# Kernel tuning notes

Measured on AMD Instinct MI355X. Metric: run time of the kernel, lower is better.

## Reference

```python
import jax, jax.numpy as jnp
import numpy as np

N, E, D, H = 50000, 800000, 128, 4
DH = D // H  # head dim = 32


def setup_inputs() -> dict:
    key = jax.random.key(0)
    ks = jax.random.split(key, 16)
    inp = {
        "node_feats": jax.random.normal(ks[0], (N, D), jnp.float32),
        "edge_feats": jax.random.normal(ks[1], (E, D), jnp.float32),
        "src": jax.random.randint(ks[2], (E,), 0, N, jnp.int32),
        "dst": jax.random.randint(ks[3], (E,), 0, N, jnp.int32),
        # MHA projections (no bias since num_input == num_output feats)
        "Wq": jax.random.normal(ks[4], (D, D), jnp.float32) / np.sqrt(D),
        "Wk": jax.random.normal(ks[5], (D, D), jnp.float32) / np.sqrt(D),
        "Wv": jax.random.normal(ks[6], (D, D), jnp.float32) / np.sqrt(D),
        "We": jax.random.normal(ks[7], (D, D), jnp.float32) / np.sqrt(D),
        # output projection (with bias)
        "O_w": jax.random.normal(ks[8], (D, D), jnp.float32) / np.sqrt(D),
        "O_b": jnp.zeros((D,), jnp.float32),
        # batch-norm affine params
        "g1n": jnp.ones((D,), jnp.float32), "b1n": jnp.zeros((D,), jnp.float32),
        "g1e": jnp.ones((D,), jnp.float32), "b1e": jnp.zeros((D,), jnp.float32),
        "g2": jnp.ones((D,), jnp.float32), "b2": jnp.zeros((D,), jnp.float32),
        # node-feats MLP (no bias)
        "W1": jax.random.normal(ks[9], (D, 2 * D), jnp.float32) / np.sqrt(D),
        "W2": jax.random.normal(ks[10], (2 * D, D), jnp.float32) / np.sqrt(2 * D),
    }
    return inp


def _batch_norm(x, gamma, beta, eps=1e-5):
    # training-style BatchNorm1d: biased variance over the batch (node/edge) dim
    mean = jnp.mean(x, axis=0)
    var = jnp.var(x, axis=0)
    return (x - mean) * jax.lax.rsqrt(var + eps) * gamma + beta


def reference(node_feats, edge_feats, src, dst, Wq, Wk, Wv, We, O_w, O_b,
              g1n, b1n, g1e, b1e, g2, b2, W1, W2):
    h_in1 = node_feats
    nf = _batch_norm(node_feats, g1n, b1n)
    ef = _batch_norm(edge_feats, g1e, b1e)

    Q = (nf @ Wq).reshape(N, H, DH)
    K = (nf @ Wk).reshape(N, H, DH)
    V = (nf @ Wv).reshape(N, H, DH)
    proj_e = (ef @ We).reshape(E, H, DH)

    # edge-wise multiplicative attention: [E, H, DH]
    score = jnp.clip(K[src] * Q[dst] / np.sqrt(DH).astype(np.float32), -5.0, 5.0) * proj_e
    s = jnp.exp(jnp.clip(jnp.sum(score, axis=-1, keepdims=True), -5.0, 5.0))  # [E, H, 1]

    # scatter-sum aggregation to destination nodes
    wV = jax.ops.segment_sum(s * V[src], dst, num_segments=N)  # [N, H, DH]
    z = jax.ops.segment_sum(s, dst, num_segments=N)            # [N, H, 1]
    h = (wV / (z + 1e-6)).reshape(N, D)

    # dropout is identity in eval mode
    h = h @ O_w + O_b
    h = h_in1 + h  # residual 1

    h_in2 = h
    h = _batch_norm(h, g2, b2)
    h = jax.nn.silu(h @ W1) @ W2  # node_feats_MLP (dropout = identity)
    h = h_in2 + h  # residual 2
    return h
```

## Files before the change

kernel.cpp:

```cpp
#include <hip/hip_runtime.h>
#include <hip/hip_bf16.h>
#include <math.h>

#define N_NODES 50000
#define N_EDGES 800000
#define DIM 128
#define NH 4

typedef __attribute__((ext_vector_type(8))) short bf16x8;
typedef __attribute__((ext_vector_type(4))) float f32x4;
typedef unsigned int uint;
typedef unsigned short ushort;

__device__ inline short f2bf(float f) {
  __hip_bfloat16 h = __float2bfloat16(f);
  return __builtin_bit_cast(short, h);
}
__device__ inline uint pack_bf2(float lo, float hi) {
  return (uint)(ushort)f2bf(lo) | ((uint)(ushort)f2bf(hi) << 16);
}
__device__ inline float bflo(uint u) { return __builtin_bit_cast(float, u << 16); }
__device__ inline float bfhi(uint u) { return __builtin_bit_cast(float, u & 0xffff0000u); }

__global__ __launch_bounds__(256) void stats_all_kernel(
    const float* __restrict__ nf, const float* __restrict__ ef,
    const int* __restrict__ dst,
    float* __restrict__ stats_n, float* __restrict__ stats_e,
    int* __restrict__ deg, ushort* __restrict__ efb) {
  __shared__ float s_sum[DIM];
  __shared__ float s_sq[DIM];
  int t = threadIdx.x;
  if (t < DIM) { s_sum[t] = 0.f; s_sq[t] = 0.f; }
  __syncthreads();
  int c4 = (t & 31) * 4;
  int rg = t >> 5;
  float sum0=0,sum1=0,sum2=0,sum3=0, sq0=0,sq1=0,sq2=0,sq3=0;
  if (blockIdx.x < 512) {
    for (long row = (long)blockIdx.x * 8 + rg; row < N_NODES; row += 512L * 8) {
      float4 v = *reinterpret_cast<const float4*>(nf + row * DIM + c4);
      sum0 += v.x; sq0 += v.x * v.x;
      sum1 += v.y; sq1 += v.y * v.y;
      sum2 += v.z; sq2 += v.z * v.z;
      sum3 += v.w; sq3 += v.w * v.w;
    }
    atomicAdd(&s_sum[c4 + 0], sum0); atomicAdd(&s_sq[c4 + 0], sq0);
    atomicAdd(&s_sum[c4 + 1], sum1); atomicAdd(&s_sq[c4 + 1], sq1);
    atomicAdd(&s_sum[c4 + 2], sum2); atomicAdd(&s_sq[c4 + 2], sq2);
    atomicAdd(&s_sum[c4 + 3], sum3); atomicAdd(&s_sq[c4 + 3], sq3);
    __syncthreads();
    if (t < DIM) {
      atomicAdd(&stats_n[t], s_sum[t]);
      atomicAdd(&stats_n[DIM + t], s_sq[t]);
    }
  } else {
    long bid2 = blockIdx.x - 512;
    for (long i = bid2 * 256 + t; i < N_EDGES; i += 2048L * 256) {
      atomicAdd(&deg[dst[i]], 1);
    }
    for (long row = bid2 * 8 + rg; row < N_EDGES; row += 2048L * 8) {
      float4 v = *reinterpret_cast<const float4*>(ef + row * DIM + c4);
      sum0 += v.x; sq0 += v.x * v.x;
      sum1 += v.y; sq1 += v.y * v.y;
      sum2 += v.z; sq2 += v.z * v.z;
      sum3 += v.w; sq3 += v.w * v.w;
      uint2 p;
      p.x = pack_bf2(v.x, v.y);
      p.y = pack_bf2(v.z, v.w);
      *reinterpret_cast<uint2*>(efb + row * DIM + c4) = p;
    }
    atomicAdd(&s_sum[c4 + 0], sum0); atomicAdd(&s_sq[c4 + 0], sq0);
    atomicAdd(&s_sum[c4 + 1], sum1); atomicAdd(&s_sq[c4 + 1], sq1);
    atomicAdd(&s_sum[c4 + 2], sum2); atomicAdd(&s_sq[c4 + 2], sq2);
    atomicAdd(&s_sum[c4 + 3], sum3); atomicAdd(&s_sq[c4 + 3], sq3);
    __syncthreads();
    if (t < DIM) {
      atomicAdd(&stats_e[t], s_sum[t]);
      atomicAdd(&stats_e[DIM + t], s_sq[t]);
    }
  }
}

__global__ __launch_bounds__(1024) void fold6_kernel(
    const float* __restrict__ Wq, const float* __restrict__ Wk,
    const float* __restrict__ Wv, const float* __restrict__ We,
    const float* __restrict__ Ow, const float* __restrict__ W2,
    const float* __restrict__ stats_n, const float* __restrict__ stats_e,
    const float* __restrict__ g1n, const float* __restrict__ b1n,
    const float* __restrict__ g1e, const float* __restrict__ b1e, float inv_s,
    short* __restrict__ WqT, short* __restrict__ WkT,
    short* __restrict__ WvT, short* __restrict__ WeT,
    short* __restrict__ OwT, short* __restrict__ W2T,
    float* __restrict__ bq, float* __restrict__ bk,
    float* __restrict__ bv, float* __restrict__ be) {
  int b = blockIdx.x;
  int t = threadIdx.x;
  if (b == 4) {
    int d = t & 127, kg = t >> 7;
#pragma unroll
    for (int j = 0; j < 16; ++j) {
      int k = kg * 16 + j;
      OwT[d * DIM + k] = f2bf(Ow[k * DIM + d]);
    }
    return;
  }
  if (b == 5) {
    int d = t & 127, kg = t >> 7;
#pragma unroll
    for (int j = 0; j < 32; ++j) {
      int k = kg * 32 + j;
      W2T[d * 256 + k] = f2bf(W2[k * DIM + d]);
    }
    return;
  }
  __shared__ float red[8][DIM];
  __shared__ float sab[DIM], sbb[DIM];
  const float* W = (b == 0) ? Wq : (b == 1) ? Wk : (b == 2) ? Wv : We;
  const float* stats = (b == 3) ? stats_e : stats_n;
  const float* gamma = (b == 3) ? g1e : g1n;
  const float* beta  = (b == 3) ? b1e : b1n;
  float M            = (b == 3) ? (float)N_EDGES : (float)N_NODES;
  float scale = (b == 1) ? inv_s : 1.f;
  short* WT = (b == 0) ? WqT : (b == 1) ? WkT : (b == 2) ? WvT : WeT;
  float* bias = (b == 0) ? bq : (b == 1) ? bk : (b == 2) ? bv : be;
  if (t < DIM) {
    float mean = stats[t] / M;
    float var = stats[DIM + t] / M - mean * mean;
    float a = gamma[t] * rsqrtf(var + 1e-5f);
    sab[t] = a;
    sbb[t] = beta[t] - mean * a;
  }
  __syncthreads();
  int d = t & 127, kg = t >> 7;
  int ct = d >> 4, lr = d & 15;
  int L = (ct >> 1) * 32 + lr * 2 + (ct & 1);
  float bacc = 0.f;
#pragma unroll
  for (int j = 0; j < 16; ++j) {
    int k = kg * 16 + j;
    float wv = W[k * DIM + L];
    WT[d * DIM + k] = f2bf(scale * sab[k] * wv);
    bacc += sbb[k] * wv;
  }
  red[kg][d] = bacc;
  __syncthreads();
  if (kg == 0) {
    float s = 0.f;
#pragma unroll
    for (int j = 0; j < 8; ++j) s += red[j][d];
    bias[d] = scale * s;
  }
}

__global__ __launch_bounds__(256) void fold_w1_kernel(
    const float* __restrict__ W1, const float* __restrict__ stats_h,
    const float* __restrict__ g2, const float* __restrict__ b2,
    short* __restrict__ W1F, float* __restrict__ bias1) {
  __shared__ float sab[DIM], sbb[DIM];
  __shared__ float red[16][17];
  int t = threadIdx.x;
  if (t < DIM) {
    float mean = stats_h[t] / (float)N_NODES;
    float var = stats_h[DIM + t] / (float)N_NODES - mean * mean;
    float a = g2[t] * rsqrtf(var + 1e-5f);
    sab[t] = a;
    sbb[t] = b2[t] - mean * a;
  }
  __syncthreads();
  int dl = t & 15, kg = t >> 4;
  int d = blockIdx.x * 16 + dl;
  float bacc = 0.f;
#pragma unroll
  for (int j = 0; j < 8; ++j) {
    int k = kg * 8 + j;
    float wv = W1[k * 256 + d];
    W1F[d * DIM + k] = f2bf(sab[k] * wv);
    bacc += sbb[k] * wv;
  }
  red[dl][kg] = bacc;
  __syncthreads();
  if (kg == 0) {
    float s = 0.f;
#pragma unroll
    for (int j = 0; j < 16; ++j) s += red[dl][j];
    bias1[d] = s;
  }
}

__device__ inline void load_a_frags(const float* __restrict__ X, long m0,
                                    int lr, int lg, bf16x8 a[4]) {
#pragma unroll
  for (int ks = 0; ks < 4; ++ks) {
    const float* p = X + (m0 + lr) * DIM + ks * 32 + lg * 8;
    float4 v0 = *reinterpret_cast<const float4*>(p);
    float4 v1 = *reinterpret_cast<const float4*>(p + 4);
    bf16x8 af;
    af[0] = f2bf(v0.x); af[1] = f2bf(v0.y); af[2] = f2bf(v0.z); af[3] = f2bf(v0.w);
    af[4] = f2bf(v1.x); af[5] = f2bf(v1.y); af[6] = f2bf(v1.z); af[7] = f2bf(v1.w);
    a[ks] = af;
  }
}

__global__ __launch_bounds__(256) void qkv_mfma_kernel(
    const float* __restrict__ nf,
    const short* __restrict__ WqT, const short* __restrict__ WkT, const short* __restrict__ WvT,
    const float* __restrict__ bq, const float* __restrict__ bk, const float* __restrict__ bv,
    ushort* __restrict__ Qb, ushort* __restrict__ Kb, ushort* __restrict__ Vb) {
  int t = threadIdx.x;
  int w = t >> 6, l = t & 63;
  int lr = l & 15, lg = l >> 4;
  long m0 = (long)blockIdx.x * 64 + w * 16;
  if (m0 >= N_NODES) return;
  bf16x8 a[4];
  load_a_frags(nf, m0, lr, lg, a);
  const short* Ws[3] = {WqT, WkT, WvT};
  const float* bs[3] = {bq, bk, bv};
  ushort* Os[3] = {Qb, Kb, Vb};
#pragma unroll 1
  for (int m = 0; m < 3; ++m) {
    const short* WT = Ws[m];
    f32x4 acc[8];
#pragma unroll
    for (int ct = 0; ct < 8; ++ct) acc[ct] = (f32x4){0.f, 0.f, 0.f, 0.f};
#pragma unroll
    for (int ct = 0; ct < 8; ++ct) {
#pragma unroll
      for (int ks = 0; ks < 4; ++ks) {
        bf16x8 b = *reinterpret_cast<const bf16x8*>(WT + (ct * 16 + lr) * DIM + ks * 32 + lg * 8);
        acc[ct] = __builtin_amdgcn_mfma_f32_16x16x32_bf16(a[ks], b, acc[ct], 0, 0, 0);
      }
    }
    const float* bb = bs[m];
    ushort* O = Os[m];
#pragma unroll
    for (int h = 0; h < 4; ++h) {
      float b0 = bb[(2 * h) * 16 + lr];
      float b1 = bb[(2 * h + 1) * 16 + lr];
#pragma unroll
      for (int r = 0; r < 4; ++r) {
        uint u = pack_bf2(acc[2 * h][r] + b0, acc[2 * h + 1][r] + b1);
        *reinterpret_cast<uint*>(O + (m0 + lg * 4 + r) * DIM + h * 32 + lr * 2) = u;
      }
    }
  }
}

#define SCAN_T 1024
#define PER_T 49
__global__ __launch_bounds__(SCAN_T) void scan_kernel(
    const int* __restrict__ deg, int* __restrict__ row_start, int* __restrict__ cursor) {
  __shared__ int ps[SCAN_T];
  int t = threadIdx.x;
  int base = t * PER_T;
  int lsum = 0;
  int local[PER_T];
#pragma unroll
  for (int j = 0; j < PER_T; ++j) {
    int idx = base + j;
    int d = (idx < N_NODES) ? deg[idx] : 0;
    local[j] = lsum;
    lsum += d;
  }
  ps[t] = lsum;
  __syncthreads();
  for (int off = 1; off < SCAN_T; off <<= 1) {
    int v = (t >= off) ? ps[t - off] : 0;
    __syncthreads();
    ps[t] += v;
    __syncthreads();
  }
  int prefix = (t == 0) ? 0 : ps[t - 1];
#pragma unroll
  for (int j = 0; j < PER_T; ++j) {
    int idx = base + j;
    if (idx < N_NODES) {
      int v = prefix + local[j];
      row_start[idx] = v;
      cursor[idx] = v;
    }
  }
  if (t == SCAN_T - 1) row_start[N_NODES] = ps[SCAN_T - 1];
}

__global__ __launch_bounds__(256) void scatter_kernel(
    const int* __restrict__ src, const int* __restrict__ dst,
    int* __restrict__ cursor, int2* __restrict__ csr) {
  int i = blockIdx.x * 256 + threadIdx.x;
  int d = dst[i];
  int pos = atomicAdd(&cursor[d], 1);
  csr[pos] = make_int2(src[i], i);
}

#define ES_GRID 2048
__global__ __launch_bounds__(256) void edge_score_kernel(
    const ushort* __restrict__ efb,
    const int* __restrict__ src, const int* __restrict__ dst,
    const short* __restrict__ WeT, const float* __restrict__ be,
    const ushort* __restrict__ Qb, const ushort* __restrict__ Kb,
    float* __restrict__ s_out) {
  const int NT = N_EDGES / 64;
  int t = threadIdx.x;
  int w = t >> 6, l = t & 63;
  int lr = l & 15, lg = l >> 4;
  float ber[8];
#pragma unroll
  for (int ct = 0; ct < 8; ++ct) ber[ct] = be[ct * 16 + lr];

  for (int tile = blockIdx.x; tile < NT; tile += gridDim.x) {
    long m0 = (long)tile * 64 + w * 16;
    long eb = m0 + lg * 4;
    int4 s4 = *reinterpret_cast<const int4*>(src + eb);
    int4 d4 = *reinterpret_cast<const int4*>(dst + eb);
    int sn[4] = {s4.x, s4.y, s4.z, s4.w};
    int dn[4] = {d4.x, d4.y, d4.z, d4.w};
    uint Kg[4][4], Qg[4][4];
#pragma unroll
    for (int r = 0; r < 4; ++r) {
#pragma unroll
      for (int h = 0; h < 4; ++h) {
        Kg[r][h] = *reinterpret_cast<const uint*>(Kb + (long)sn[r] * DIM + h * 32 + lr * 2);
        Qg[r][h] = *reinterpret_cast<const uint*>(Qb + (long)dn[r] * DIM + h * 32 + lr * 2);
      }
    }
    bf16x8 a[4];
#pragma unroll
    for (int ks = 0; ks < 4; ++ks) {
      a[ks] = *reinterpret_cast<const bf16x8*>(efb + (m0 + lr) * DIM + ks * 32 + lg * 8);
    }
    f32x4 acc[8];
#pragma unroll
    for (int ct = 0; ct < 8; ++ct) acc[ct] = (f32x4){0.f, 0.f, 0.f, 0.f};
#pragma unroll
    for (int ct = 0; ct < 8; ++ct) {
#pragma unroll
      for (int ks = 0; ks < 4; ++ks) {
        bf16x8 b = *reinterpret_cast<const bf16x8*>(WeT + (ct * 16 + lr) * DIM + ks * 32 + lg * 8);
        acc[ct] = __builtin_amdgcn_mfma_f32_16x16x32_bf16(a[ks], b, acc[ct], 0, 0, 0);
      }
    }
#pragma unroll
    for (int r = 0; r < 4; ++r) {
      float hs0, hs1, hs2, hs3;
      {
        float h0, h1, h2, h3;
#pragma unroll
        for (int h = 0; h < 4; ++h) {
          float k0 = bflo(Kg[r][h]), k1 = bfhi(Kg[r][h]);
          float q0 = bflo(Qg[r][h]), q1 = bfhi(Qg[r][h]);
          float pe0 = acc[2 * h][r] + ber[2 * h];
          float pe1 = acc[2 * h + 1][r] + ber[2 * h + 1];
          float v = fminf(fmaxf(k0 * q0, -5.f), 5.f) * pe0
                  + fminf(fmaxf(k1 * q1, -5.f), 5.f) * pe1;
          if (h == 0) h0 = v; else if (h == 1) h1 = v; else if (h == 2) h2 = v; else h3 = v;
        }
        hs0 = h0; hs1 = h1; hs2 = h2; hs3 = h3;
      }
#pragma unroll
      for (int m2 = 8; m2 >= 1; m2 >>= 1) {
        hs0 += __shfl_xor(hs0, m2);
        hs1 += __shfl_xor(hs1, m2);
        hs2 += __shfl_xor(hs2, m2);
        hs3 += __shfl_xor(hs3, m2);
      }
      if (lr < 4) {
        float myh = (lr == 0) ? hs0 : ((lr == 1) ? hs1 : ((lr == 2) ? hs2 : hs3));
        s_out[(eb + r) * 4 + lr] = __expf(fminf(fmaxf(myh, -5.f), 5.f));
      }
    }
  }
}

__global__ __launch_bounds__(256) void aggregate_kernel(
    const int* __restrict__ row_start, const int2* __restrict__ csr,
    const float* __restrict__ s_arr, const ushort* __restrict__ Vb,
    ushort* __restrict__ haggb) {
  int t = threadIdx.x;
  int w = t >> 6, l = t & 63;
  int n = blockIdx.x * 4 + w;
  int r0 = row_start[n], r1 = row_start[n + 1];
  int h = l >> 4;
  float a0 = 0.f, a1 = 0.f, zacc = 0.f;
  int idx = r0;
  for (; idx + 4 <= r1; idx += 4) {
    int2 rec[4];
#pragma unroll
    for (int j = 0; j < 4; ++j) rec[j] = csr[idx + j];
    float sv[4]; uint uv[4];
#pragma unroll
    for (int j = 0; j < 4; ++j) {
      sv[j] = s_arr[(long)rec[j].y * 4 + h];
      uv[j] = *reinterpret_cast<const uint*>(Vb + (long)rec[j].x * DIM + l * 2);
    }
#pragma unroll
    for (int j = 0; j < 4; ++j) {
      a0 += sv[j] * bflo(uv[j]);
      a1 += sv[j] * bfhi(uv[j]);
      zacc += sv[j];
    }
  }
  for (; idx < r1; ++idx) {
    int2 ra = csr[idx];
    float sa = s_arr[(long)ra.y * 4 + h];
    uint ua = *reinterpret_cast<const uint*>(Vb + (long)ra.x * DIM + l * 2);
    a0 += sa * bflo(ua);
    a1 += sa * bfhi(ua);
    zacc += sa;
  }
  float inv = 1.f / (zacc + 1e-6f);
  *reinterpret_cast<uint*>(haggb + (long)n * DIM + l * 2) = pack_bf2(a0 * inv, a1 * inv);
}

__global__ __launch_bounds__(256) void attnout_mfma_kernel(
    const ushort* __restrict__ haggb, const short* __restrict__ OwT,
    const float* __restrict__ Ob, const float* __restrict__ h_in1,
    float* __restrict__ hres, float* __restrict__ stats2) {
  int t = threadIdx.x;
  int w = t >> 6, l = t & 63;
  int lr = l & 15, lg = l >> 4;
  long m0 = (long)blockIdx.x * 64 + w * 16;
  if (m0 >= N_NODES) return;
  bf16x8 a[4];
#pragma unroll
  for (int ks = 0; ks < 4; ++ks) {
    a[ks] = *reinterpret_cast<const bf16x8*>(haggb + (m0 + lr) * DIM + ks * 32 + lg * 8);
  }
  f32x4 acc[8];
#pragma unroll
  for (int ct = 0; ct < 8; ++ct) acc[ct] = (f32x4){0.f, 0.f, 0.f, 0.f};
#pragma unroll
  for (int ct = 0; ct < 8; ++ct) {
#pragma unroll
    for (int ks = 0; ks < 4; ++ks) {
      bf16x8 b = *reinterpret_cast<const bf16x8*>(OwT + (ct * 16 + lr) * DIM + ks * 32 + lg * 8);
      acc[ct] = __builtin_amdgcn_mfma_f32_16x16x32_bf16(a[ks], b, acc[ct], 0, 0, 0);
    }
  }
#pragma unroll
  for (int ct = 0; ct < 8; ++ct) {
    float ob = Ob[ct * 16 + lr];
    float ls = 0.f, lq = 0.f;
#pragma unroll
    for (int r = 0; r < 4; ++r) {
      long idx = (m0 + lg * 4 + r) * DIM + ct * 16 + lr;
      float hv = h_in1[idx] + acc[ct][r] + ob;
      hres[idx] = hv;
      ls += hv; lq += hv * hv;
    }
    ls += __shfl_xor(ls, 16); ls += __shfl_xor(ls, 32);
    lq += __shfl_xor(lq, 16); lq += __shfl_xor(lq, 32);
    if (lg == 0) {
      atomicAdd(&stats2[ct * 16 + lr], ls);
      atomicAdd(&stats2[DIM + ct * 16 + lr], lq);
    }
  }
}

__global__ __launch_bounds__(256) void mlp_mfma_kernel(
    const float* __restrict__ hres, const short* __restrict__ W1F,
    const float* __restrict__ bias1, const short* __restrict__ W2T,
    float* __restrict__ out) {
  __shared__ short mid[64][264];
  int t = threadIdx.x;
  int w = t >> 6, l = t & 63;
  int lr = l & 15, lg = l >> 4;
  long m0 = (long)blockIdx.x * 64 + w * 16;
  if (m0 >= N_NODES) return;
  bf16x8 a1[4];
  load_a_frags(hres, m0, lr, lg, a1);
#pragma unroll
  for (int ct = 0; ct < 16; ++ct) {
    f32x4 acc = (f32x4){0.f, 0.f, 0.f, 0.f};
#pragma unroll
    for (int ks = 0; ks < 4; ++ks) {
      bf16x8 b = *reinterpret_cast<const bf16x8*>(W1F + (ct * 16 + lr) * DIM + ks * 32 + lg * 8);
      acc = __builtin_amdgcn_mfma_f32_16x16x32_bf16(a1[ks], b, acc, 0, 0, 0);
    }
    float bb = bias1[ct * 16 + lr];
#pragma unroll
    for (int r = 0; r < 4; ++r) {
      float x = acc[r] + bb;
      float sl = x / (1.f + __expf(-x));
      mid[w * 16 + lg * 4 + r][ct * 16 + lr] = f2bf(sl);
    }
  }
  bf16x8 a2[8];
#pragma unroll
  for (int ks = 0; ks < 8; ++ks) {
    a2[ks] = *reinterpret_cast<const bf16x8*>(&mid[w * 16 + lr][ks * 32 + lg * 8]);
  }
#pragma unroll
  for (int ct = 0; ct < 8; ++ct) {
    f32x4 acc = (f32x4){0.f, 0.f, 0.f, 0.f};
#pragma unroll
    for (int ks = 0; ks < 8; ++ks) {
      bf16x8 b = *reinterpret_cast<const bf16x8*>(W2T + (ct * 16 + lr) * 256 + ks * 32 + lg * 8);
      acc = __builtin_amdgcn_mfma_f32_16x16x32_bf16(a2[ks], b, acc, 0, 0, 0);
    }
#pragma unroll
    for (int r = 0; r < 4; ++r) {
      long idx = (m0 + lg * 4 + r) * DIM + ct * 16 + lr;
      out[idx] = hres[idx] + acc[r];
    }
  }
}

extern "C" void kernel_launch(void* const* d_in, const int* in_sizes, int n_in,
                              void* d_out, int out_size, void* d_ws, size_t ws_size,
                              hipStream_t stream) {
  const float* node_feats = (const float*)d_in[0];
  const float* edge_feats = (const float*)d_in[1];
  const int* src = (const int*)d_in[2];
  const int* dst = (const int*)d_in[3];
  const float* Wq = (const float*)d_in[4];
  const float* Wk = (const float*)d_in[5];
  const float* Wv = (const float*)d_in[6];
  const float* We = (const float*)d_in[7];
  const float* Ow = (const float*)d_in[8];
  const float* Ob = (const float*)d_in[9];
  const float* g1n = (const float*)d_in[10];
  const float* b1n = (const float*)d_in[11];
  const float* g1e = (const float*)d_in[12];
  const float* b1e = (const float*)d_in[13];
  const float* g2 = (const float*)d_in[14];
  const float* b2 = (const float*)d_in[15];
  const float* W1 = (const float*)d_in[16];
  const float* W2 = (const float*)d_in[17];
  float* out = (float*)d_out;
  float* w = (float*)d_ws;

  float* stats_n = w + 0;
  float* stats_e = w + 256;
  float* stats_h = w + 512;
  float* bq = w + 1536;
  float* bk = w + 1664;
  float* bv = w + 1792;
  float* be = w + 1920;
  short* WqT = (short*)(w + 2048);
  short* WkT = (short*)(w + 10240);
  short* WvT = (short*)(w + 18432);
  short* WeT = (short*)(w + 26624);
  short* OwT = (short*)(w + 34816);
  short* W1F = (short*)(w + 43008);
  short* W2T = (short*)(w + 59392);
  float* bias1 = w + 75776;
  ushort* Qb = (ushort*)(w + 76032);
  ushort* Kb = (ushort*)(w + 3276032);
  ushort* Vb = (ushort*)(w + 6476032);
  float* s_arr = w + 9676032;
  int* deg = (int*)(w + 12876032);
  int* row_start = deg + 50048;
  int* cursor = row_start + 50064;
  int2* csr = (int2*)(cursor + 50048);
  ushort* efb = (ushort*)(w + 16226192);
  ushort* haggb = (ushort*)(w + 76032);

  const float inv_s = 0.17677669529663687f;

  hipMemsetAsync(w, 0, 768 * sizeof(float), stream);
  hipMemsetAsync(deg, 0, 50000 * sizeof(int), stream);

  stats_all_kernel<<<2560, 256, 0, stream>>>(
      node_feats, edge_feats, dst, stats_n, stats_e, deg, efb);
  fold6_kernel<<<6, 1024, 0, stream>>>(Wq, Wk, Wv, We, Ow, W2, stats_n, stats_e,
                                       g1n, b1n, g1e, b1e, inv_s,
                                       WqT, WkT, WvT, WeT, OwT, W2T, bq, bk, bv, be);
  scan_kernel<<<1, SCAN_T, 0, stream>>>(deg, row_start, cursor);
  scatter_kernel<<<N_EDGES / 256, 256, 0, stream>>>(src, dst, cursor, csr);

  qkv_mfma_kernel<<<(N_NODES + 63) / 64, 256, 0, stream>>>(
      node_feats, WqT, WkT, WvT, bq, bk, bv, Qb, Kb, Vb);
  edge_score_kernel<<<ES_GRID, 256, 0, stream>>>(
      efb, src, dst, WeT, be, Qb, Kb, s_arr);
  aggregate_kernel<<<N_NODES / 4, 256, 0, stream>>>(row_start, csr, s_arr, Vb, haggb);
  attnout_mfma_kernel<<<(N_NODES + 63) / 64, 256, 0, stream>>>(
      haggb, OwT, Ob, node_feats, out, stats_h);
  fold_w1_kernel<<<16, 256, 0, stream>>>(W1, stats_h, g2, b2, W1F, bias1);
  mlp_mfma_kernel<<<(N_NODES + 63) / 64, 256, 0, stream>>>(out, W1F, bias1, W2T, out);
}
```

Before: 815.2 us.

## Merge scan into fold kernel and scatter into QKV kernel to cut launches

Moves the degree prefix-scan into an extra block of the weight-fold kernel, and merges the CSR scatter with the QKV projection kernel by giving the scatter its own extra blocks. This removes two kernel launches and lets the independent scatter and GEMM work share the GPU at the same time. It also switches the edge-feature loads in edge_score to nontemporal loads and raises wave priority around the MFMA loop. The heterogeneous block roles can imbalance scheduling, and the scan now runs as a single block of the fold launch.

```diff
diff --git a/kernel.cpp b/kernel.cpp
--- a/kernel.cpp
+++ b/kernel.cpp
@@ -80,7 +80,9 @@
   }
 }
 
-__global__ __launch_bounds__(1024) void fold6_kernel(
+#define SCAN_T 1024
+#define PER_T 49
+__global__ __launch_bounds__(1024) void fold7_kernel(
     const float* __restrict__ Wq, const float* __restrict__ Wk,
     const float* __restrict__ Wv, const float* __restrict__ We,
     const float* __restrict__ Ow, const float* __restrict__ W2,
@@ -91,9 +93,44 @@
     short* __restrict__ WvT, short* __restrict__ WeT,
     short* __restrict__ OwT, short* __restrict__ W2T,
     float* __restrict__ bq, float* __restrict__ bk,
-    float* __restrict__ bv, float* __restrict__ be) {
+    float* __restrict__ bv, float* __restrict__ be,
+    const int* __restrict__ deg, int* __restrict__ row_start,
+    int* __restrict__ cursor) {
   int b = blockIdx.x;
   int t = threadIdx.x;
+  if (b == 6) {
+    __shared__ int ps[SCAN_T];
+    int base = t * PER_T;
+    int lsum = 0;
+    int local[PER_T];
+#pragma unroll
+    for (int j = 0; j < PER_T; ++j) {
+      int idx = base + j;
+      int d = (idx < N_NODES) ? deg[idx] : 0;
+      local[j] = lsum;
+      lsum += d;
+    }
+    ps[t] = lsum;
+    __syncthreads();
+    for (int off = 1; off < SCAN_T; off <<= 1) {
+      int v = (t >= off) ? ps[t - off] : 0;
+      __syncthreads();
+      ps[t] += v;
+      __syncthreads();
+    }
+    int prefix = (t == 0) ? 0 : ps[t - 1];
+#pragma unroll
+    for (int j = 0; j < PER_T; ++j) {
+      int idx = base + j;
+      if (idx < N_NODES) {
+        int v = prefix + local[j];
+        row_start[idx] = v;
+        cursor[idx] = v;
+      }
+    }
+    if (t == SCAN_T - 1) row_start[N_NODES] = ps[SCAN_T - 1];
+    return;
+  }
   if (b == 4) {
     int d = t & 127, kg = t >> 7;
 #pragma unroll
@@ -200,12 +237,22 @@
   }
 }
 
-__global__ __launch_bounds__(256) void qkv_mfma_kernel(
+#define QKV_BLOCKS 782
+__global__ __launch_bounds__(256) void scatter_qkv_kernel(
     const float* __restrict__ nf,
     const short* __restrict__ WqT, const short* __restrict__ WkT, const short* __restrict__ WvT,
     const float* __restrict__ bq, const float* __restrict__ bk, const float* __restrict__ bv,
-    ushort* __restrict__ Qb, ushort* __restrict__ Kb, ushort* __restrict__ Vb) {
-  int t = threadIdx.x;
+    ushort* __restrict__ Qb, ushort* __restrict__ Kb, ushort* __restrict__ Vb,
+    const int* __restrict__ src, const int* __restrict__ dst,
+    int* __restrict__ cursor, int2* __restrict__ csr) {
+  int t = threadIdx.x;
+  if (blockIdx.x >= QKV_BLOCKS) {
+    int i = (blockIdx.x - QKV_BLOCKS) * 256 + t;
+    int d = dst[i];
+    int pos = atomicAdd(&cursor[d], 1);
+    csr[pos] = make_int2(src[i], i);
+    return;
+  }
   int w = t >> 6, l = t & 63;
   int lr = l & 15, lg = l >> 4;
   long m0 = (long)blockIdx.x * 64 + w * 16;
@@ -244,52 +291,6 @@
   }
 }
 
-#define SCAN_T 1024
-#define PER_T 49
-__global__ __launch_bounds__(SCAN_T) void scan_kernel(
-    const int* __restrict__ deg, int* __restrict__ row_start, int* __restrict__ cursor) {
-  __shared__ int ps[SCAN_T];
-  int t = threadIdx.x;
-  int base = t * PER_T;
-  int lsum = 0;
-  int local[PER_T];
-#pragma unroll
-  for (int j = 0; j < PER_T; ++j) {
-    int idx = base + j;
-    int d = (idx < N_NODES) ? deg[idx] : 0;
-    local[j] = lsum;
-    lsum += d;
-  }
-  ps[t] = lsum;
-  __syncthreads();
-  for (int off = 1; off < SCAN_T; off <<= 1) {
-    int v = (t >= off) ? ps[t - off] : 0;
-    __syncthreads();
-    ps[t] += v;
-    __syncthreads();
-  }
-  int prefix = (t == 0) ? 0 : ps[t - 1];
-#pragma unroll
-  for (int j = 0; j < PER_T; ++j) {
-    int idx = base + j;
-    if (idx < N_NODES) {
-      int v = prefix + local[j];
-      row_start[idx] = v;
-      cursor[idx] = v;
-    }
-  }
-  if (t == SCAN_T - 1) row_start[N_NODES] = ps[SCAN_T - 1];
-}
-
-__global__ __launch_bounds__(256) void scatter_kernel(
-    const int* __restrict__ src, const int* __restrict__ dst,
-    int* __restrict__ cursor, int2* __restrict__ csr) {
-  int i = blockIdx.x * 256 + threadIdx.x;
-  int d = dst[i];
-  int pos = atomicAdd(&cursor[d], 1);
-  csr[pos] = make_int2(src[i], i);
-}
-
 #define ES_GRID 2048
 __global__ __launch_bounds__(256) void edge_score_kernel(
     const ushort* __restrict__ efb,
@@ -324,11 +325,13 @@
     bf16x8 a[4];
 #pragma unroll
     for (int ks = 0; ks < 4; ++ks) {
-      a[ks] = *reinterpret_cast<const bf16x8*>(efb + (m0 + lr) * DIM + ks * 32 + lg * 8);
+      a[ks] = __builtin_nontemporal_load(
+          reinterpret_cast<const bf16x8*>(efb + (m0 + lr) * DIM + ks * 32 + lg * 8));
     }
     f32x4 acc[8];
 #pragma unroll
     for (int ct = 0; ct < 8; ++ct) acc[ct] = (f32x4){0.f, 0.f, 0.f, 0.f};
+    __builtin_amdgcn_s_setprio(1);
 #pragma unroll
     for (int ct = 0; ct < 8; ++ct) {
 #pragma unroll
@@ -337,6 +340,7 @@
         acc[ct] = __builtin_amdgcn_mfma_f32_16x16x32_bf16(a[ks], b, acc[ct], 0, 0, 0);
       }
     }
+    __builtin_amdgcn_s_setprio(0);
 #pragma unroll
     for (int r = 0; r < 4; ++r) {
       float hs0, hs1, hs2, hs3;
@@ -560,14 +564,12 @@
 
   stats_all_kernel<<<2560, 256, 0, stream>>>(
       node_feats, edge_feats, dst, stats_n, stats_e, deg, efb);
-  fold6_kernel<<<6, 1024, 0, stream>>>(Wq, Wk, Wv, We, Ow, W2, stats_n, stats_e,
+  fold7_kernel<<<7, 1024, 0, stream>>>(Wq, Wk, Wv, We, Ow, W2, stats_n, stats_e,
                                        g1n, b1n, g1e, b1e, inv_s,
-                                       WqT, WkT, WvT, WeT, OwT, W2T, bq, bk, bv, be);
-  scan_kernel<<<1, SCAN_T, 0, stream>>>(deg, row_start, cursor);
-  scatter_kernel<<<N_EDGES / 256, 256, 0, stream>>>(src, dst, cursor, csr);
-
-  qkv_mfma_kernel<<<(N_NODES + 63) / 64, 256, 0, stream>>>(
-      node_feats, WqT, WkT, WvT, bq, bk, bv, Qb, Kb, Vb);
+                                       WqT, WkT, WvT, WeT, OwT, W2T, bq, bk, bv, be,
+                                       deg, row_start, cursor);
+  scatter_qkv_kernel<<<QKV_BLOCKS + N_EDGES / 256, 256, 0, stream>>>(
+      node_feats, WqT, WkT, WvT, bq, bk, bv, Qb, Kb, Vb, src, dst, cursor, csr);
   edge_score_kernel<<<ES_GRID, 256, 0, stream>>>(
       efb, src, dst, WeT, be, Qb, Kb, s_arr);
   aggregate_kernel<<<N_NODES / 4, 256, 0, stream>>>(row_start, csr, s_arr, Vb, haggb);
```

After: 732.5 us. 1.11x faster.
